# Performance work log

Hardware: AMD Instinct MI355X
Metric: run time of the kernel (lower is better)

Reference implementation:

```python
import jax, jax.numpy as jnp
import numpy as np

C = 1.0  # Poincare ball curvature
EPS = 1e-15


def setup_inputs() -> dict:
    key = jax.random.key(0)
    k1, k2, k3 = jax.random.split(key, 3)
    B, S, D_IN, D_OUT = 16, 8192, 128, 128
    # points strictly inside the unit ball: ||x|| ~ 0.05*sqrt(128) ~ 0.57
    x = 0.05 * jax.random.normal(k1, (B, S, D_IN), dtype=jnp.float32)
    z = 0.01 * jax.random.normal(k2, (D_IN, D_OUT), dtype=jnp.float32)  # init_std=0.01 normal
    r = 0.01 * jax.random.normal(k3, (D_OUT,), dtype=jnp.float32)
    return {"x": x, "z": z, "r": r}


def reference(x, z, r):
    # Poincare MLR (Shimizu et al., Hyperbolic NN++), as in hypll PoincareBall.mlr
    c = jnp.asarray(C, x.dtype)
    cs = jnp.sqrt(c)
    prefix = x.shape[:-1]
    x2 = x.reshape(-1, x.shape[-1])                       # [N, d_in]
    # conformal factor lambda_x = 2 / (1 - c ||x||^2)
    lam = 2.0 / (1.0 - c * jnp.sum(x2 * x2, axis=-1, keepdims=True))  # [N, 1]
    z_norm = jnp.maximum(jnp.linalg.norm(z, axis=0), EPS)             # [d_out]
    two_csr = 2.0 * cs * r                                            # [d_out]
    inner = x2 @ z                                                    # [N, d_out]
    arg = (cs * lam * inner / z_norm) * jnp.cosh(two_csr) - (lam - 1.0) * jnp.sinh(two_csr)
    out = (2.0 * z_norm / cs) * jnp.arcsinh(arg)                      # [N, d_out]
    return out.reshape(*prefix, z.shape[1])
```

## Files before the change

kernel.cpp:

```cpp
#include <hip/hip_runtime.h>
#include <cstdint>


typedef __attribute__((ext_vector_type(8))) short short8;
typedef __attribute__((ext_vector_type(4))) float floatx4;

#define D 128

__device__ inline unsigned bf16_rhu(float f) {
    return (__float_as_uint(f) + 0x8000u) >> 16;
}
__device__ inline unsigned pack2(float lo, float hi) {
    return bf16_rhu(lo) | (bf16_rhu(hi) << 16);
}

__global__ void hmlr_prep(const float* __restrict__ z, const float* __restrict__ r,
                          unsigned short* __restrict__ zt_sw, float4* __restrict__ abs4) {
    int n = blockIdx.x;
    int k = threadIdx.x;
    float v = z[k * D + n];
    int c = k >> 3, p = k & 7;
    zt_sw[n * D + ((c ^ (n & 7)) << 3) + p] = (unsigned short)bf16_rhu(v);
    float pw = v * v;
    #pragma unroll
    for (int off = 32; off >= 1; off >>= 1) pw += __shfl_down(pw, off, 64);
    __shared__ float tmp[2];
    if ((k & 63) == 0) tmp[k >> 6] = pw;
    __syncthreads();
    if (k == 0) {
        float ss = tmp[0] + tmp[1];
        float zn = fmaxf(sqrtf(ss), 1e-15f);
        float tc = 2.0f * r[n];
        abs4[n] = make_float4(coshf(tc) / zn, sinhf(tc),
                              2.0f * zn * 0.69314718055994531f, 0.0f);
    }
}

__global__ __launch_bounds__(256, 5) void hmlr_main(const float* __restrict__ x,
                                                    const unsigned short* __restrict__ zt_sw,
                                                    const float4* __restrict__ abs4,
                                                    float* __restrict__ out) {
    __shared__ __align__(16) unsigned char lds[32768];

    const int t    = threadIdx.x;
    const int w    = t >> 6;
    const int l    = t & 63;
    const int quad = l >> 4;
    const int l15  = l & 15;
    const int l7   = l & 7;

#if __has_builtin(__builtin_amdgcn_global_load_lds)
    #pragma unroll
    for (int i = 0; i < 8; ++i) {
        int ci = w * 512 + i * 64 + l;
        __builtin_amdgcn_global_load_lds(
            (const __attribute__((address_space(1))) unsigned int*)(zt_sw + (ci << 3)),
            (__attribute__((address_space(3))) unsigned int*)(lds + ((w * 512 + i * 64) << 4)),
            16, 0, 0);
    }
#else
    #pragma unroll
    for (int i = 0; i < 8; ++i) {
        int ci = w * 512 + i * 64 + l;
        *reinterpret_cast<uint4*>(&lds[ci << 4]) = reinterpret_cast<const uint4*>(zt_sw)[ci];
    }
#endif
    __syncthreads();

    const int rowbase = blockIdx.x * 64 + w * 16;
    const float* xrow = x + (size_t)(rowbase + l15) * D + (quad << 3);
    float4 xv[8];
    #pragma unroll
    for (int kc = 0; kc < 4; ++kc) {
        xv[2 * kc]     = *reinterpret_cast<const float4*>(xrow + (kc << 5));
        xv[2 * kc + 1] = *reinterpret_cast<const float4*>(xrow + (kc << 5) + 4);
    }

    float ssq = 0.f;
    #pragma unroll
    for (int i = 0; i < 8; ++i)
        ssq += xv[i].x * xv[i].x + xv[i].y * xv[i].y + xv[i].z * xv[i].z + xv[i].w * xv[i].w;
    ssq += __shfl_xor(ssq, 16);
    ssq += __shfl_xor(ssq, 32);

    short8 afrag[4];
    #pragma unroll
    for (int kc = 0; kc < 4; ++kc) {
        union { short8 s8; unsigned u[4]; } af;
        af.u[0] = pack2(xv[2 * kc].x,     xv[2 * kc].y);
        af.u[1] = pack2(xv[2 * kc].z,     xv[2 * kc].w);
        af.u[2] = pack2(xv[2 * kc + 1].x, xv[2 * kc + 1].y);
        af.u[3] = pack2(xv[2 * kc + 1].z, xv[2 * kc + 1].w);
        afrag[kc] = af.s8;
    }

    floatx4 acc[8];
    #pragma unroll
    for (int nt = 0; nt < 8; ++nt) acc[nt] = (floatx4){0.f, 0.f, 0.f, 0.f};

    #pragma unroll
    for (int kc = 0; kc < 4; ++kc) {
        short8 b[8];
        #pragma unroll
        for (int nt = 0; nt < 8; ++nt)
            b[nt] = *reinterpret_cast<const short8*>(
                &lds[((nt * 16 + l15) << 8) + (((quad + (kc << 2)) ^ l7) << 4)]);
        #pragma unroll
        for (int nt = 0; nt < 8; ++nt)
            acc[nt] = __builtin_amdgcn_mfma_f32_16x16x32_bf16(afrag[kc], b[nt], acc[nt], 0, 0, 0);
    }

    float4 cst[8];
    #pragma unroll
    for (int nt = 0; nt < 8; ++nt) cst[nt] = abs4[nt * 16 + l15];

    #pragma unroll
    for (int reg = 0; reg < 4; ++reg) {
        float rss = __shfl(ssq, (quad << 2) | reg);
        float lam = 2.0f / (1.0f - rss);
        float lm1 = lam - 1.0f;
        float* orow = out + (size_t)(rowbase + (quad << 2) + reg) * D + l15;
        #pragma unroll
        for (int nt = 0; nt < 8; ++nt) {
            float arg = __fmaf_rn(lam * acc[nt][reg], cst[nt].x, -lm1 * cst[nt].y);
            float a   = fabsf(arg);
            float as  = __log2f(a + __fsqrt_rn(__fmaf_rn(a, a, 1.0f)));
            orow[nt * 16] = copysignf(as, arg) * cst[nt].z;
        }
    }
}

extern "C" void kernel_launch(void* const* d_in, const int* in_sizes, int n_in,
                              void* d_out, int out_size, void* d_ws, size_t ws_size,
                              hipStream_t stream) {
    const float* x = (const float*)d_in[0];
    const float* z = (const float*)d_in[1];
    const float* r = (const float*)d_in[2];
    float* out = (float*)d_out;

    char* wsb = (char*)d_ws;
    unsigned short* zt_sw = (unsigned short*)wsb;
    float4* abs4 = (float4*)(wsb + 128 * D * sizeof(unsigned short));

    hmlr_prep<<<128, 128, 0, stream>>>(z, r, zt_sw, abs4);

    const int n_rows = in_sizes[0] / D;
    hmlr_main<<<n_rows / 64, 256, 0, stream>>>(x, zt_sw, abs4, out);
}
```

Baseline: 120.5 us.

## Swap MFMA operands for row-contiguous float4 stores and hoist x loads

Swaps the MFMA A/B operands so each lane's accumulator holds four consecutive output columns of one row. The epilogue can then write float4 vectors instead of scalar strided stores, and the per-row lambda is computed directly without shuffles. Per-column constants move to a struct-of-arrays layout so they can be read as float4. The x global loads are issued before the LDS fill and barrier so their latency overlaps the z staging.

```diff
diff --git a/kernel.cpp b/kernel.cpp
--- a/kernel.cpp
+++ b/kernel.cpp
@@ -15,7 +15,7 @@
 }
 
 __global__ void hmlr_prep(const float* __restrict__ z, const float* __restrict__ r,
-                          unsigned short* __restrict__ zt_sw, float4* __restrict__ abs4) {
+                          unsigned short* __restrict__ zt_sw, float* __restrict__ cabc) {
     int n = blockIdx.x;
     int k = threadIdx.x;
     float v = z[k * D + n];
@@ -31,14 +31,22 @@
         float ss = tmp[0] + tmp[1];
         float zn = fmaxf(sqrtf(ss), 1e-15f);
         float tc = 2.0f * r[n];
-        abs4[n] = make_float4(coshf(tc) / zn, sinhf(tc),
-                              2.0f * zn * 0.69314718055994531f, 0.0f);
+        cabc[n]           = coshf(tc) / zn;
+        cabc[D + n]       = sinhf(tc);
+        cabc[2 * D + n]   = 2.0f * zn * 0.69314718055994531f;
     }
+}
+
+__device__ inline float mlr_elem(float v, float lam, float lm1, float A, float B, float S) {
+    float arg = __fmaf_rn(lam * v, A, -lm1 * B);
+    float a   = fabsf(arg);
+    float as  = __log2f(a + __fsqrt_rn(__fmaf_rn(a, a, 1.0f)));
+    return copysignf(as, arg) * S;
 }
 
 __global__ __launch_bounds__(256, 5) void hmlr_main(const float* __restrict__ x,
                                                     const unsigned short* __restrict__ zt_sw,
-                                                    const float4* __restrict__ abs4,
+                                                    const float* __restrict__ cabc,
                                                     float* __restrict__ out) {
     __shared__ __align__(16) unsigned char lds[32768];
 
@@ -48,6 +56,15 @@
     const int quad = l >> 4;
     const int l15  = l & 15;
     const int l7   = l & 7;
+
+    const int rowbase = blockIdx.x * 64 + w * 16;
+    const float* xrow = x + (size_t)(rowbase + l15) * D + (quad << 3);
+    float4 xv[8];
+    #pragma unroll
+    for (int kc = 0; kc < 4; ++kc) {
+        xv[2 * kc]     = *reinterpret_cast<const float4*>(xrow + (kc << 5));
+        xv[2 * kc + 1] = *reinterpret_cast<const float4*>(xrow + (kc << 5) + 4);
+    }
 
 #if __has_builtin(__builtin_amdgcn_global_load_lds)
     #pragma unroll
@@ -65,16 +82,6 @@
         *reinterpret_cast<uint4*>(&lds[ci << 4]) = reinterpret_cast<const uint4*>(zt_sw)[ci];
     }
 #endif
-    __syncthreads();
-
-    const int rowbase = blockIdx.x * 64 + w * 16;
-    const float* xrow = x + (size_t)(rowbase + l15) * D + (quad << 3);
-    float4 xv[8];
-    #pragma unroll
-    for (int kc = 0; kc < 4; ++kc) {
-        xv[2 * kc]     = *reinterpret_cast<const float4*>(xrow + (kc << 5));
-        xv[2 * kc + 1] = *reinterpret_cast<const float4*>(xrow + (kc << 5) + 4);
-    }
 
     float ssq = 0.f;
     #pragma unroll
@@ -83,7 +90,7 @@
     ssq += __shfl_xor(ssq, 16);
     ssq += __shfl_xor(ssq, 32);
 
-    short8 afrag[4];
+    short8 xfrag[4];
     #pragma unroll
     for (int kc = 0; kc < 4; ++kc) {
         union { short8 s8; unsigned u[4]; } af;
@@ -91,8 +98,10 @@
         af.u[1] = pack2(xv[2 * kc].z,     xv[2 * kc].w);
         af.u[2] = pack2(xv[2 * kc + 1].x, xv[2 * kc + 1].y);
         af.u[3] = pack2(xv[2 * kc + 1].z, xv[2 * kc + 1].w);
-        afrag[kc] = af.s8;
+        xfrag[kc] = af.s8;
     }
+
+    __syncthreads();
 
     floatx4 acc[8];
     #pragma unroll
@@ -100,33 +109,35 @@
 
     #pragma unroll
     for (int kc = 0; kc < 4; ++kc) {
-        short8 b[8];
+        short8 zf[8];
         #pragma unroll
         for (int nt = 0; nt < 8; ++nt)
-            b[nt] = *reinterpret_cast<const short8*>(
+            zf[nt] = *reinterpret_cast<const short8*>(
                 &lds[((nt * 16 + l15) << 8) + (((quad + (kc << 2)) ^ l7) << 4)]);
         #pragma unroll
         for (int nt = 0; nt < 8; ++nt)
-            acc[nt] = __builtin_amdgcn_mfma_f32_16x16x32_bf16(afrag[kc], b[nt], acc[nt], 0, 0, 0);
+            acc[nt] = __builtin_amdgcn_mfma_f32_16x16x32_bf16(zf[nt], xfrag[kc], acc[nt], 0, 0, 0);
     }
 
-    float4 cst[8];
-    #pragma unroll
-    for (int nt = 0; nt < 8; ++nt) cst[nt] = abs4[nt * 16 + l15];
+    const float lam = 2.0f / (1.0f - ssq);
+    const float lm1 = lam - 1.0f;
+    float* orow = out + (size_t)(rowbase + l15) * D + (quad << 2);
+    const float4* cAp = reinterpret_cast<const float4*>(cabc);
+    const float4* cBp = reinterpret_cast<const float4*>(cabc + D);
+    const float4* cSp = reinterpret_cast<const float4*>(cabc + 2 * D);
 
     #pragma unroll
-    for (int reg = 0; reg < 4; ++reg) {
-        float rss = __shfl(ssq, (quad << 2) | reg);
-        float lam = 2.0f / (1.0f - rss);
-        float lm1 = lam - 1.0f;
-        float* orow = out + (size_t)(rowbase + (quad << 2) + reg) * D + l15;
-        #pragma unroll
-        for (int nt = 0; nt < 8; ++nt) {
-            float arg = __fmaf_rn(lam * acc[nt][reg], cst[nt].x, -lm1 * cst[nt].y);
-            float a   = fabsf(arg);
-            float as  = __log2f(a + __fsqrt_rn(__fmaf_rn(a, a, 1.0f)));
-            orow[nt * 16] = copysignf(as, arg) * cst[nt].z;
-        }
+    for (int nt = 0; nt < 8; ++nt) {
+        int cb4 = (nt << 2) + quad;
+        float4 A4 = cAp[cb4];
+        float4 B4 = cBp[cb4];
+        float4 S4 = cSp[cb4];
+        float4 o;
+        o.x = mlr_elem(acc[nt][0], lam, lm1, A4.x, B4.x, S4.x);
+        o.y = mlr_elem(acc[nt][1], lam, lm1, A4.y, B4.y, S4.y);
+        o.z = mlr_elem(acc[nt][2], lam, lm1, A4.z, B4.z, S4.z);
+        o.w = mlr_elem(acc[nt][3], lam, lm1, A4.w, B4.w, S4.w);
+        *reinterpret_cast<float4*>(orow + (nt << 4)) = o;
     }
 }
 
@@ -140,10 +151,10 @@
 
     char* wsb = (char*)d_ws;
     unsigned short* zt_sw = (unsigned short*)wsb;
-    float4* abs4 = (float4*)(wsb + 128 * D * sizeof(unsigned short));
+    float* cabc = (float*)(wsb + 128 * D * sizeof(unsigned short));
 
-    hmlr_prep<<<128, 128, 0, stream>>>(z, r, zt_sw, abs4);
+    hmlr_prep<<<128, 128, 0, stream>>>(z, r, zt_sw, cabc);
 
     const int n_rows = in_sizes[0] / D;
-    hmlr_main<<<n_rows / 64, 256, 0, stream>>>(x, zt_sw, abs4, out);
+    hmlr_main<<<n_rows / 64, 256, 0, stream>>>(x, zt_sw, cabc, out);
 }
```

After: 125.7 us. 1.04x slower.
